# Performance work log

Hardware: AMD Instinct MI355X
Metric: run time of the kernel (lower is better)

Reference implementation:

```python
import jax, jax.numpy as jnp
import numpy as np

B, T, C = 4, 2048, 1024
N_HEAD = 16
HEAD = C // N_HEAD

def setup_inputs() -> dict:
    key = jax.random.key(0)
    k1, k2, k3 = jax.random.split(key, 3)
    x = jax.random.normal(k1, (B, T, C), dtype=jnp.float32)
    w_attn = jax.random.normal(k2, (C, 3 * C), dtype=jnp.float32) * (1.0 / np.sqrt(C))
    w_proj = jax.random.normal(k3, (C, C), dtype=jnp.float32) * (1.0 / np.sqrt(C))
    return {"x": x, "w_attn": w_attn, "w_proj": w_proj}

def reference(x, w_attn, w_proj):
    b, t, c = x.shape
    qkv = x @ w_attn  # [B,T,3C]
    q, k, v = jnp.split(qkv, 3, axis=-1)
    # [B,T,C] -> [B,H,T,D]
    def heads(z):
        return z.reshape(b, t, N_HEAD, HEAD).transpose(0, 2, 1, 3)
    q, k, v = heads(q), heads(k), heads(v)
    scale = 1.0 / np.sqrt(HEAD)
    att = jnp.einsum('bhqd,bhkd->bhqk', q, k) * scale  # [B,H,T,T]
    causal = jnp.tril(jnp.ones((t, t), dtype=bool))
    att = jnp.where(causal[None, None], att, -jnp.inf)
    att = jax.nn.softmax(att, axis=-1)
    y = jnp.einsum('bhqk,bhkd->bhqd', att, v)  # [B,H,T,D]
    y = y.transpose(0, 2, 1, 3).reshape(b, t, c)
    return y @ w_proj
```

## Files before the change

### kernel.cpp

```cpp
#include <hip/hip_runtime.h>
#include <hip/hip_bf16.h>


typedef __attribute__((ext_vector_type(8))) short bf16x8;
typedef __attribute__((ext_vector_type(4))) float f32x4;
typedef __attribute__((ext_vector_type(16))) float f32x16;

#define T_DIM 2048
#define NHEAD 16
#define HDIM  64

__device__ __forceinline__ unsigned short f2bf(float f) {
    union { float f; unsigned int u; } v; v.f = f;
    unsigned int r = v.u + 0x7fffu + ((v.u >> 16) & 1u);
    return (unsigned short)(r >> 16);
}

__device__ __forceinline__ unsigned cvtpk_bf16(float lo, float hi) {
    unsigned r;
    asm("v_cvt_pk_bf16_f32 %0, %1, %2" : "=v"(r) : "v"(lo), "v"(hi));
    return r;
}
__device__ __forceinline__ void pl32swap(unsigned &x, unsigned &y) {
    asm("v_permlane32_swap_b32 %0, %1" : "+v"(x), "+v"(y));
}
__device__ __forceinline__ bf16x8 mk8(unsigned w0, unsigned w1, unsigned w2, unsigned w3) {
    union { unsigned u[4]; bf16x8 v; } p;
    p.u[0] = w0; p.u[1] = w1; p.u[2] = w2; p.u[3] = w3;
    return p.v;
}

__device__ __forceinline__ void gload_lds16(const void* g, void* l) {
    __builtin_amdgcn_global_load_lds(
        (const __attribute__((address_space(1))) void*)g,
        (__attribute__((address_space(3))) void*)l,
        16, 0, 0);
}

__global__ void cvt_bf16_k(const float* __restrict__ src, unsigned short* __restrict__ dst, int n) {
    int i = (blockIdx.x * blockDim.x + threadIdx.x) * 4;
    if (i < n) {
        float4 v = *(const float4*)(src + i);
        ushort4 o; o.x = f2bf(v.x); o.y = f2bf(v.y); o.z = f2bf(v.z); o.w = f2bf(v.w);
        *(ushort4*)(dst + i) = o;
    }
}

__global__ void transpose_wb_k(const float* __restrict__ src, unsigned short* __restrict__ dst,
                               int R, int Cc) {
    __shared__ float tile[32][33];
    int c0 = blockIdx.x * 32, r0 = blockIdx.y * 32;
    int tx = threadIdx.x & 31, ty = threadIdx.x >> 5;
    #pragma unroll
    for (int i = 0; i < 32; i += 8)
        tile[ty + i][tx] = src[(size_t)(r0 + ty + i) * Cc + c0 + tx];
    __syncthreads();
    #pragma unroll
    for (int i = 0; i < 32; i += 8)
        dst[(size_t)(c0 + ty + i) * R + r0 + tx] = f2bf(tile[tx][ty + i]);
}

template<int EPI>
__global__ __launch_bounds__(256) void gemm_bt_k(
    const unsigned short* __restrict__ A, const unsigned short* __restrict__ Bt,
    void* __restrict__ out0, void* __restrict__ out1, void* __restrict__ out2,
    int M, int N, int K)
{
    __shared__ __align__(16) unsigned short smem[16384];
    unsigned short* sA = smem;
    unsigned short* sB = smem + 8192;

    const int tid = threadIdx.x, lane = tid & 63, wave = tid >> 6;
    const int wm = wave >> 1, wn = wave & 1;
    const int lrow = lane & 15, hi = lane >> 4;

    const int nwg = gridDim.x * gridDim.y;
    const int lin = blockIdx.y * gridDim.x + blockIdx.x;
    const int lin2 = (lin & 7) * (nwg >> 3) + (lin >> 3);
    const int bxg = lin2 % gridDim.x, byg = lin2 / gridDim.x;
    const int row0 = byg * 128, col0 = bxg * 128;

    const int arow = tid >> 3;
    const int gk = ((tid & 7) ^ (arow & 7)) * 8;
    const unsigned short* gA = A  + (size_t)(row0 + arow) * K + gk;
    const unsigned short* gB = Bt + (size_t)(col0 + arow) * K + gk;

    const int NT = K >> 6;

#define STAGE(t) { const size_t ko_ = (size_t)(t) * 64; \
        gload_lds16(gA + ko_,                   sA + tid * 8); \
        gload_lds16(gA + (size_t)32 * K + ko_,  sA + (tid + 256) * 8); \
        gload_lds16(gA + (size_t)64 * K + ko_,  sA + (tid + 512) * 8); \
        gload_lds16(gA + (size_t)96 * K + ko_,  sA + (tid + 768) * 8); \
        gload_lds16(gB + ko_,                   sB + tid * 8); \
        gload_lds16(gB + (size_t)32 * K + ko_,  sB + (tid + 256) * 8); \
        gload_lds16(gB + (size_t)64 * K + ko_,  sB + (tid + 512) * 8); \
        gload_lds16(gB + (size_t)96 * K + ko_,  sB + (tid + 768) * 8); }

    f32x4 acc[4][4] = {};

    for (int t = 0; t < NT; ++t) {
        STAGE(t);
        __syncthreads();
        bf16x8 af[2][4], bf_[2][4];
        #pragma unroll
        for (int ks = 0; ks < 2; ++ks) {
            const int kc = (ks * 4 + hi) ^ (lrow & 7);
            #pragma unroll
            for (int mi = 0; mi < 4; ++mi)
                af[ks][mi] = *(const bf16x8*)&sA[((wm * 64 + mi * 16 + lrow) * 8 + kc) * 8];
            #pragma unroll
            for (int ni = 0; ni < 4; ++ni)
                bf_[ks][ni] = *(const bf16x8*)&sB[((wn * 64 + ni * 16 + lrow) * 8 + kc) * 8];
        }
        __builtin_amdgcn_s_setprio(1);
        #pragma unroll
        for (int ks = 0; ks < 2; ++ks)
            #pragma unroll
            for (int mi = 0; mi < 4; ++mi)
                #pragma unroll
                for (int ni = 0; ni < 4; ++ni)
                    acc[mi][ni] = __builtin_amdgcn_mfma_f32_16x16x32_bf16(af[ks][mi], bf_[ks][ni], acc[mi][ni], 0, 0, 0);
        __builtin_amdgcn_s_setprio(0);
        __syncthreads();
    }
#undef STAGE

    if (EPI == 1) {
        #pragma unroll
        for (int mi = 0; mi < 4; ++mi)
            #pragma unroll
            for (int ni = 0; ni < 4; ++ni) {
                int gm0 = row0 + wm * 64 + mi * 16 + hi * 4;
                int gn  = col0 + wn * 64 + ni * 16 + lrow;
                #pragma unroll
                for (int r = 0; r < 4; ++r)
                    ((float*)out0)[(size_t)(gm0 + r) * N + gn] = acc[mi][ni][r];
            }
    } else if (col0 < 1024) {
        const int bb = row0 >> 11;
        #pragma unroll
        for (int mi = 0; mi < 4; ++mi)
            #pragma unroll
            for (int ni = 0; ni < 4; ++ni) {
                int gm0 = row0 + wm * 64 + mi * 16 + hi * 4;
                int gn  = col0 + wn * 64 + ni * 16 + lrow;
                int h = (gn >> 6) & 15, d = gn & 63;
                #pragma unroll
                for (int r = 0; r < 4; ++r) {
                    int t = (gm0 + r) & 2047;
                    ((unsigned short*)out0)[((size_t)(bb * NHEAD + h) * T_DIM + t) * HDIM + d] =
                        f2bf(acc[mi][ni][r] * 0.18033688011112042f);
                }
            }
    } else {
        const bool isK = (col0 < 2048);
        __syncthreads();
        #pragma unroll
        for (int mi = 0; mi < 4; ++mi) {
            #pragma unroll
            for (int ni = 0; ni < 4; ++ni) {
                const int gnl = wn * 64 + ni * 16 + lrow;
                const int hl = gnl >> 6, d = gnl & 63;
                #pragma unroll
                for (int r = 0; r < 4; ++r) {
                    const int tl = wm * 64 + mi * 16 + hi * 4 + r;
                    int idx;
                    if (isK) idx = (hl * 2 + (tl >> 6)) * 4096 + ((d >> 3) * 64 + (tl & 63)) * 8 + (d & 7);
                    else     idx = (hl * 2 + (tl >> 6)) * 4096 + (((tl >> 3) & 7) * 64 + d) * 8 + (tl & 7);
                    smem[idx] = f2bf(acc[mi][ni][r]);
                }
            }
        }
        __syncthreads();
        unsigned short* outb = (unsigned short*)(isK ? out1 : out2);
        const int bb = row0 >> 11;
        const int h0 = ((col0 - (isK ? 1024 : 2048)) >> 6);
        const int tc0 = (row0 & 2047) >> 6;
        #pragma unroll
        for (int seg = 0; seg < 4; ++seg) {
            const int hl = seg >> 1, tc = seg & 1;
            const size_t gbase = ((size_t)(bb * NHEAD + h0 + hl) * 32 + tc0 + tc) * 4096;
            *(uint4*)(outb + gbase + tid * 8)         = *(const uint4*)(smem + seg * 4096 + tid * 8);
            *(uint4*)(outb + gbase + (tid + 256) * 8) = *(const uint4*)(smem + seg * 4096 + (tid + 256) * 8);
        }
    }
}

__global__ __launch_bounds__(512) void attn_k(
    const unsigned short* __restrict__ qb, const unsigned short* __restrict__ kcm,
    const unsigned short* __restrict__ vcm, unsigned short* __restrict__ yb)
{
    __shared__ __align__(16) unsigned short Ks[2][4096];
    __shared__ __align__(16) unsigned short Vs[2][4096];

    const int tid = threadIdx.x, lane = tid & 63, wave = tid >> 6;
    const int bh = blockIdx.y;
    const int q32 = lane & 31, hi32 = lane >> 5;
    const unsigned short* Kg = kcm + (size_t)bh * 32 * 4096;
    const unsigned short* Vg = vcm + (size_t)bh * 32 * 4096;

    const int bxx = (blockIdx.y & 32) ? (int)blockIdx.x : 7 - (int)blockIdx.x;
    const int ntiles = 4 * bxx + 4;
    const int q0w = bxx * 256 + wave * 32;
    const int qg = q0w + q32;

    const unsigned short* qrow = qb + ((size_t)bh * T_DIM + q0w + q32) * HDIM;
    bf16x8 qf[4];
    #pragma unroll
    for (int kc = 0; kc < 4; ++kc)
        qf[kc] = *(const bf16x8*)(qrow + kc * 16 + hi32 * 8);

    f32x16 o0 = {}, o1 = {};
    float lsum = 0.f;

    gload_lds16(Kg + tid * 8, &Ks[0][tid * 8]);
    gload_lds16(Vg + tid * 8, &Vs[0][tid * 8]);
    __syncthreads();

    int cur = 0;
    for (int jt = 0; jt < ntiles; ++jt) {
        if (jt + 1 < ntiles) {
            gload_lds16(Kg + (size_t)(jt + 1) * 4096 + tid * 8, &Ks[cur ^ 1][tid * 8]);
            gload_lds16(Vg + (size_t)(jt + 1) * 4096 + tid * 8, &Vs[cur ^ 1][tid * 8]);
        }
        if (jt * 64 <= q0w + 31) {
            f32x16 s0 = {}, s1 = {};
            #pragma unroll
            for (int kc = 0; kc < 4; ++kc) {
                bf16x8 a0 = *(const bf16x8*)&Ks[cur][((kc * 2 + hi32) * 64 + q32) * 8];
                bf16x8 a1 = *(const bf16x8*)&Ks[cur][((kc * 2 + hi32) * 64 + 32 + q32) * 8];
                s0 = __builtin_amdgcn_mfma_f32_32x32x16_bf16(a0, qf[kc], s0, 0, 0, 0);
                s1 = __builtin_amdgcn_mfma_f32_32x32x16_bf16(a1, qf[kc], s1, 0, 0, 0);
            }
            if (jt * 64 + 63 > q0w) {
                #pragma unroll
                for (int r = 0; r < 16; ++r) {
                    int kv0 = jt * 64 + (r & 3) + 8 * (r >> 2) + 4 * hi32;
                    if (kv0 > qg)      s0[r] = -1e30f;
                    if (kv0 + 32 > qg) s1[r] = -1e30f;
                }
            }
            bf16x8 pa[4];
            #pragma unroll
            for (int blk = 0; blk < 2; ++blk) {
                float p_[16]; unsigned w_[8];
                #pragma unroll
                for (int i = 0; i < 16; ++i) {
                    float sv = blk ? s1[i] : s0[i];
                    p_[i] = __builtin_amdgcn_exp2f(sv - 16.0f);
                    lsum += p_[i];
                }
                #pragma unroll
                for (int i = 0; i < 8; ++i) w_[i] = cvtpk_bf16(p_[2 * i], p_[2 * i + 1]);
                pl32swap(w_[0], w_[2]); pl32swap(w_[1], w_[3]);
                pl32swap(w_[4], w_[6]); pl32swap(w_[5], w_[7]);
                pa[blk * 2]     = mk8(w_[0], w_[1], w_[2], w_[3]);
                pa[blk * 2 + 1] = mk8(w_[4], w_[5], w_[6], w_[7]);
            }
            #pragma unroll
            for (int kvc = 0; kvc < 4; ++kvc) {
                bf16x8 b0 = *(const bf16x8*)&Vs[cur][((kvc * 2 + hi32) * 64 + q32) * 8];
                bf16x8 b1 = *(const bf16x8*)&Vs[cur][((kvc * 2 + hi32) * 64 + 32 + q32) * 8];
                o0 = __builtin_amdgcn_mfma_f32_32x32x16_bf16(pa[kvc], b0, o0, 0, 0, 0);
                o1 = __builtin_amdgcn_mfma_f32_32x32x16_bf16(pa[kvc], b1, o1, 0, 0, 0);
            }
        }
        __syncthreads();
        cur ^= 1;
    }

    {
        unsigned la = __float_as_uint(lsum), lb = __float_as_uint(lsum);
        pl32swap(la, lb);
        lsum = __uint_as_float(la) + __uint_as_float(lb);
    }
    const int bb2 = bh >> 4, h = bh & 15;
    #pragma unroll
    for (int r = 0; r < 16; ++r) {
        const int cr = (r & 3) + 8 * (r >> 2) + 4 * hi32;
        float inv = 1.0f / __shfl(lsum, cr);
        int t = q0w + cr;
        size_t off = ((size_t)(bb2 * T_DIM + t)) * 1024 + h * HDIM + q32;
        yb[off]      = f2bf(o0[r] * inv);
        yb[off + 32] = f2bf(o1[r] * inv);
    }
}

extern "C" void kernel_launch(void* const* d_in, const int* in_sizes, int n_in,
                              void* d_out, int out_size, void* d_ws, size_t ws_size,
                              hipStream_t stream) {
    const float* x      = (const float*)d_in[0];
    const float* w_attn = (const float*)d_in[1];
    const float* w_proj = (const float*)d_in[2];
    float* out = (float*)d_out;

    unsigned short* xb  = (unsigned short*)d_ws;
    unsigned short* wat = xb  + (size_t)8192 * 1024;
    unsigned short* wpt = wat + (size_t)3072 * 1024;
    unsigned short* qb  = wpt + (size_t)1024 * 1024;
    unsigned short* kcm = qb  + (size_t)64 * 2048 * 64;
    unsigned short* vcm = kcm + (size_t)64 * 2048 * 64;
    unsigned short* yb  = vcm + (size_t)64 * 2048 * 64;

    cvt_bf16_k<<<8192, 256, 0, stream>>>(x, xb, 8192 * 1024);
    transpose_wb_k<<<dim3(96, 32), 256, 0, stream>>>(w_attn, wat, 1024, 3072);
    transpose_wb_k<<<dim3(32, 32), 256, 0, stream>>>(w_proj, wpt, 1024, 1024);

    gemm_bt_k<0><<<dim3(24, 64), 256, 0, stream>>>(xb, wat, qb, kcm, vcm, 8192, 3072, 1024);
    attn_k<<<dim3(8, 64), 512, 0, stream>>>(qb, kcm, vcm, yb);
    gemm_bt_k<1><<<dim3(8, 64), 256, 0, stream>>>(yb, wpt, out, nullptr, nullptr, 8192, 1024, 1024);
}
```

Before: 164.2 us.

## Drop LDS staging in attention, read K/V directly from global per wave

The attention kernel no longer stages K/V tiles into shared memory with double buffering and block-wide barriers. Each wave now loads its K and V fragments straight from global memory and loops only over its own causal tile count. Blocks shrink from 512 to 256 threads, the grid doubles, and the reversed-order pairing of blocks changes. This removes the barriers and idle waves that waited on the longest wave in a block, but it repeats global/L2 reads of K/V across waves and loses the prefetch overlap.

```diff
diff --git a/kernel.cpp b/kernel.cpp
--- a/kernel.cpp
+++ b/kernel.cpp
@@ -187,22 +187,19 @@
     }
 }
 
-__global__ __launch_bounds__(512) void attn_k(
+__global__ __launch_bounds__(256) void attn_k(
     const unsigned short* __restrict__ qb, const unsigned short* __restrict__ kcm,
     const unsigned short* __restrict__ vcm, unsigned short* __restrict__ yb)
 {
-    __shared__ __align__(16) unsigned short Ks[2][4096];
-    __shared__ __align__(16) unsigned short Vs[2][4096];
-
     const int tid = threadIdx.x, lane = tid & 63, wave = tid >> 6;
     const int bh = blockIdx.y;
     const int q32 = lane & 31, hi32 = lane >> 5;
     const unsigned short* Kg = kcm + (size_t)bh * 32 * 4096;
     const unsigned short* Vg = vcm + (size_t)bh * 32 * 4096;
 
-    const int bxx = (blockIdx.y & 32) ? (int)blockIdx.x : 7 - (int)blockIdx.x;
-    const int ntiles = 4 * bxx + 4;
-    const int q0w = bxx * 256 + wave * 32;
+    const int bxx = ((blockIdx.y >> 4) & 1) ? (int)blockIdx.x : 15 - (int)blockIdx.x;
+    const int ntiles = 2 * bxx + 2;
+    const int q0w = bxx * 128 + wave * 32;
     const int qg = q0w + q32;
 
     const unsigned short* qrow = qb + ((size_t)bh * T_DIM + q0w + q32) * HDIM;
@@ -214,61 +211,57 @@
     f32x16 o0 = {}, o1 = {};
     float lsum = 0.f;
 
-    gload_lds16(Kg + tid * 8, &Ks[0][tid * 8]);
-    gload_lds16(Vg + tid * 8, &Vs[0][tid * 8]);
-    __syncthreads();
-
-    int cur = 0;
-    for (int jt = 0; jt < ntiles; ++jt) {
-        if (jt + 1 < ntiles) {
-            gload_lds16(Kg + (size_t)(jt + 1) * 4096 + tid * 8, &Ks[cur ^ 1][tid * 8]);
-            gload_lds16(Vg + (size_t)(jt + 1) * 4096 + tid * 8, &Vs[cur ^ 1][tid * 8]);
-        }
-        if (jt * 64 <= q0w + 31) {
-            f32x16 s0 = {}, s1 = {};
-            #pragma unroll
-            for (int kc = 0; kc < 4; ++kc) {
-                bf16x8 a0 = *(const bf16x8*)&Ks[cur][((kc * 2 + hi32) * 64 + q32) * 8];
-                bf16x8 a1 = *(const bf16x8*)&Ks[cur][((kc * 2 + hi32) * 64 + 32 + q32) * 8];
-                s0 = __builtin_amdgcn_mfma_f32_32x32x16_bf16(a0, qf[kc], s0, 0, 0, 0);
-                s1 = __builtin_amdgcn_mfma_f32_32x32x16_bf16(a1, qf[kc], s1, 0, 0, 0);
-            }
-            if (jt * 64 + 63 > q0w) {
-                #pragma unroll
-                for (int r = 0; r < 16; ++r) {
-                    int kv0 = jt * 64 + (r & 3) + 8 * (r >> 2) + 4 * hi32;
-                    if (kv0 > qg)      s0[r] = -1e30f;
-                    if (kv0 + 32 > qg) s1[r] = -1e30f;
-                }
-            }
-            bf16x8 pa[4];
-            #pragma unroll
-            for (int blk = 0; blk < 2; ++blk) {
-                float p_[16]; unsigned w_[8];
-                #pragma unroll
-                for (int i = 0; i < 16; ++i) {
-                    float sv = blk ? s1[i] : s0[i];
-                    p_[i] = __builtin_amdgcn_exp2f(sv - 16.0f);
-                    lsum += p_[i];
-                }
-                #pragma unroll
-                for (int i = 0; i < 8; ++i) w_[i] = cvtpk_bf16(p_[2 * i], p_[2 * i + 1]);
-                pl32swap(w_[0], w_[2]); pl32swap(w_[1], w_[3]);
-                pl32swap(w_[4], w_[6]); pl32swap(w_[5], w_[7]);
-                pa[blk * 2]     = mk8(w_[0], w_[1], w_[2], w_[3]);
-                pa[blk * 2 + 1] = mk8(w_[4], w_[5], w_[6], w_[7]);
-            }
-            #pragma unroll
-            for (int kvc = 0; kvc < 4; ++kvc) {
-                bf16x8 b0 = *(const bf16x8*)&Vs[cur][((kvc * 2 + hi32) * 64 + q32) * 8];
-                bf16x8 b1 = *(const bf16x8*)&Vs[cur][((kvc * 2 + hi32) * 64 + 32 + q32) * 8];
-                o0 = __builtin_amdgcn_mfma_f32_32x32x16_bf16(pa[kvc], b0, o0, 0, 0, 0);
-                o1 = __builtin_amdgcn_mfma_f32_32x32x16_bf16(pa[kvc], b1, o1, 0, 0, 0);
-            }
-        }
-        __syncthreads();
-        cur ^= 1;
-    }
+    const int myntiles = (q0w >> 6) + 1;
+    for (int jt = 0; jt < myntiles; ++jt) {
+        const unsigned short* Kt = Kg + (size_t)jt * 4096;
+        const unsigned short* Vt = Vg + (size_t)jt * 4096;
+
+        f32x16 s0 = {}, s1 = {};
+        #pragma unroll
+        for (int kc = 0; kc < 4; ++kc) {
+            bf16x8 a0 = *(const bf16x8*)(Kt + ((kc * 2 + hi32) * 64 + q32) * 8);
+            bf16x8 a1 = *(const bf16x8*)(Kt + ((kc * 2 + hi32) * 64 + 32 + q32) * 8);
+            s0 = __builtin_amdgcn_mfma_f32_32x32x16_bf16(a0, qf[kc], s0, 0, 0, 0);
+            s1 = __builtin_amdgcn_mfma_f32_32x32x16_bf16(a1, qf[kc], s1, 0, 0, 0);
+        }
+        bf16x8 vb0[4], vb1[4];
+        #pragma unroll
+        for (int kvc = 0; kvc < 4; ++kvc) {
+            vb0[kvc] = *(const bf16x8*)(Vt + ((kvc * 2 + hi32) * 64 + q32) * 8);
+            vb1[kvc] = *(const bf16x8*)(Vt + ((kvc * 2 + hi32) * 64 + 32 + q32) * 8);
+        }
+        if (jt * 64 + 63 > q0w) {
+            #pragma unroll
+            for (int r = 0; r < 16; ++r) {
+                int kv0 = jt * 64 + (r & 3) + 8 * (r >> 2) + 4 * hi32;
+                if (kv0 > qg)      s0[r] = -1e30f;
+                if (kv0 + 32 > qg) s1[r] = -1e30f;
+            }
+        }
+        bf16x8 pa[4];
+        #pragma unroll
+        for (int blk = 0; blk < 2; ++blk) {
+            float p_[16]; unsigned w_[8];
+            #pragma unroll
+            for (int i = 0; i < 16; ++i) {
+                float sv = blk ? s1[i] : s0[i];
+                p_[i] = __builtin_amdgcn_exp2f(sv - 16.0f);
+                lsum += p_[i];
+            }
+            #pragma unroll
+            for (int i = 0; i < 8; ++i) w_[i] = cvtpk_bf16(p_[2 * i], p_[2 * i + 1]);
+            pl32swap(w_[0], w_[2]); pl32swap(w_[1], w_[3]);
+            pl32swap(w_[4], w_[6]); pl32swap(w_[5], w_[7]);
+            pa[blk * 2]     = mk8(w_[0], w_[1], w_[2], w_[3]);
+            pa[blk * 2 + 1] = mk8(w_[4], w_[5], w_[6], w_[7]);
+        }
+        #pragma unroll
+        for (int kvc = 0; kvc < 4; ++kvc) {
+            o0 = __builtin_amdgcn_mfma_f32_32x32x16_bf16(pa[kvc], vb0[kvc], o0, 0, 0, 0);
+            o1 = __builtin_amdgcn_mfma_f32_32x32x16_bf16(pa[kvc], vb1[kvc], o1, 0, 0, 0);
+        }
+    }
+    (void)ntiles;
 
     {
         unsigned la = __float_as_uint(lsum), lb = __float_as_uint(lsum);
@@ -308,6 +301,6 @@
     transpose_wb_k<<<dim3(32, 32), 256, 0, stream>>>(w_proj, wpt, 1024, 1024);
 
     gemm_bt_k<0><<<dim3(24, 64), 256, 0, stream>>>(xb, wat, qb, kcm, vcm, 8192, 3072, 1024);
-    attn_k<<<dim3(8, 64), 512, 0, stream>>>(qb, kcm, vcm, yb);
+    attn_k<<<dim3(16, 64), 256, 0, stream>>>(qb, kcm, vcm, yb);
     gemm_bt_k<1><<<dim3(8, 64), 256, 0, stream>>>(yb, wpt, out, nullptr, nullptr, 8192, 1024, 1024);
 }
```

New measurement: 187.1 us. 14.0% more time.
